# Kernel optimization log

Measured on AMD Instinct MI355X. Metric: run time of the kernel, lower is better.

The kernel has to match this reference:

```python
import jax, jax.numpy as jnp
import numpy as np

NUM_LAYER = 5
EMB_DIM = 128
N_NODES = 50000
N_EDGES = 600000
BN_EPS = 1e-5


def setup_inputs() -> dict:
    key = jax.random.key(0)
    ks = jax.random.split(key, 16)
    d, L = EMB_DIM, NUM_LAYER
    s = 0.05
    inp = {
        "x": jax.random.randint(ks[0], (N_NODES, 3), 0, 3),
        "edge_index": jax.random.randint(ks[1], (2, N_EDGES), 0, N_NODES),
        "edge_attr": jax.random.randint(ks[2], (N_EDGES, 2), 0, 4),
        # node-feature embedding tables
        "atom_emb": jax.random.normal(ks[3], (120, d)) * s,
        "chir_emb": jax.random.normal(ks[4], (3, d)) * s,
        "hyb_emb": jax.random.normal(ks[5], (7, d)) * s,
        # per-layer GIN params, stacked over layers
        "e1": jax.random.normal(ks[6], (L, 6, d)) * s,   # bond-type edge emb
        "e2": jax.random.normal(ks[7], (L, 4, d)) * s,   # bond-direction edge emb
        "W1": jax.random.normal(ks[8], (L, d, 2 * d)) * s,
        "b1": jnp.zeros((L, 2 * d)),
        "W2": jax.random.normal(ks[9], (L, 2 * d, d)) * s,
        "b2": jnp.zeros((L, d)),
        "gamma": jnp.ones((L, d)),
        "beta": jnp.zeros((L, d)),
    }
    return inp


def _gnn_forward(x, edge_index, edge_attr, atom_emb, chir_emb, hyb_emb,
                 e1, e2, W1, b1, W2, b2, gamma, beta):
    src, dst = edge_index[0], edge_index[1]
    # input node embedding: sum of three categorical embeddings -> [N, d]
    h = atom_emb[x[:, 0]] + chir_emb[x[:, 1]] + hyb_emb[x[:, 2]]
    for l in range(NUM_LAYER):
        # per-edge embedding fused from two categorical tables -> [E, d]
        ee = e1[l][edge_attr[:, 0]] + e2[l][edge_attr[:, 1]]
        # gather source features, add edge emb, scatter-add to destination
        msg = h[src] + ee                                  # [E, d]
        agg = jax.ops.segment_sum(msg, dst, num_segments=N_NODES)  # [N, d]
        # GIN MLP: Linear(d,2d) -> ReLU -> Linear(2d,d)
        h2 = jax.nn.relu(agg @ W1[l] + b1[l]) @ W2[l] + b2[l]
        # BatchNorm1d (training-mode batch statistics, biased var)
        mu = h2.mean(axis=0)
        var = h2.var(axis=0)
        h2 = gamma[l] * (h2 - mu) * jax.lax.rsqrt(var + BN_EPS) + beta[l]
        # ReLU on all but the last layer (dropout is identity in eval)
        h = h2 if l == NUM_LAYER - 1 else jax.nn.relu(h2)
    return h


def reference(x, edge_index, edge_attr, atom_emb, chir_emb, hyb_emb,
              e1, e2, W1, b1, W2, b2, gamma, beta):
    return _gnn_forward(x, edge_index, edge_attr, atom_emb, chir_emb, hyb_emb,
                        e1, e2, W1, b1, W2, b2, gamma, beta)
```

## Files before the change

kernel.cpp:

```cpp
#include <hip/hip_runtime.h>
#include <hip/hip_bf16.h>

#define NN 50000
#define NE 600000
#define D 128
#define NL 5
#define AGG_BLOCKS 2048
#define AGG_WAVES (AGG_BLOCKS * 4)

typedef __hip_bfloat16 bf16;
typedef unsigned short ushort_t;
typedef _Float16 half_t;
typedef __attribute__((ext_vector_type(8))) _Float16 half8;
typedef __attribute__((ext_vector_type(4))) _Float16 half4;
typedef __attribute__((ext_vector_type(8))) short short8;
typedef __attribute__((ext_vector_type(4))) float f32x4;
typedef __attribute__((ext_vector_type(2))) float f32x2;

__device__ __forceinline__ float b2f(bf16 v) { return __bfloat162float(v); }

__device__ __forceinline__ float loadF(const void* p, long long i, int isf32) {
    if (isf32) return ((const float*)p)[i];
    return b2f(((const bf16*)p)[i]);
}

__global__ void detect_k(const void* __restrict__ atom, int* __restrict__ flag) {
    __shared__ int vote;
    if (threadIdx.x == 0) vote = 0;
    __syncthreads();
    unsigned short u = ((const unsigned short*)atom)[threadIdx.x];
    unsigned short ex = (u >> 7) & 0xFF;
    if (ex >= 0x90) atomicOr(&vote, 1);
    __syncthreads();
    if (threadIdx.x == 0) *flag = vote;
}

__global__ void zero_f(float* __restrict__ p, int n) {
    int i = blockIdx.x * 256 + threadIdx.x;
    if (i < n) p[i] = 0.f;
}
__global__ void zero_i(int* __restrict__ p, int n) {
    int i = blockIdx.x * 256 + threadIdx.x;
    if (i < n) p[i] = 0;
}

__global__ void prepw_k(const void* __restrict__ W1, const void* __restrict__ W2,
                        const void* __restrict__ e1, const void* __restrict__ e2,
                        const int* __restrict__ fl,
                        half_t* __restrict__ w1t, half_t* __restrict__ w2t,
                        float* __restrict__ combT) {
    int isf32 = *fl;
    int idx = blockIdx.x * 256 + threadIdx.x;
    const int per = NL * 2 * D * D;
    if (idx < per) {
        int l = idx / (2 * D * D);
        int r = idx % (2 * D * D);
        int n = r >> 7, k = r & 127;
        w1t[idx] = (half_t)loadF(W1, (long long)l * 2 * D * D + (long long)k * 256 + n, isf32);
    } else if (idx < 2 * per) {
        int j = idx - per;
        int l = j / (2 * D * D);
        int r = j % (2 * D * D);
        int n = r >> 8, k = r & 255;
        w2t[j] = (half_t)loadF(W2, (long long)l * 2 * D * D + (long long)k * D + n, isf32);
    } else if (idx < 2 * per + NL * 24 * D) {
        int j = idx - 2 * per;
        int l = j / (24 * D);
        int r = j % (24 * D);
        int c = r >> 7, f = r & 127;
        combT[j] = loadF(e1, (long long)l * 6 * D + (long long)(c >> 2) * D + f, isf32) +
                   loadF(e2, (long long)l * 4 * D + (long long)(c & 3) * D + f, isf32);
    }
}

__global__ void hist_k(const int* __restrict__ ei, int* __restrict__ deg) {
    int e = blockIdx.x * 256 + threadIdx.x;
    if (e < NE) atomicAdd(&deg[ei[NE + e]], 1);
}

__global__ void scan1_k(const int* __restrict__ deg, int* __restrict__ tmp,
                        int* __restrict__ partial) {
    __shared__ int s[256];
    int t = threadIdx.x;
    int i = blockIdx.x * 256 + t;
    int v = (i < NN) ? deg[i] : 0;
    s[t] = v;
    __syncthreads();
    for (int off = 1; off < 256; off <<= 1) {
        int x = (t >= off) ? s[t - off] : 0;
        __syncthreads();
        s[t] += x;
        __syncthreads();
    }
    if (i < NN) tmp[i] = s[t];
    if (t == 255) partial[blockIdx.x] = s[255];
}

__global__ void scan2_k(int* __restrict__ partial, int nb) {
    __shared__ int s[256];
    int t = threadIdx.x;
    int v = (t < nb) ? partial[t] : 0;
    s[t] = v;
    __syncthreads();
    for (int off = 1; off < 256; off <<= 1) {
        int x = (t >= off) ? s[t - off] : 0;
        __syncthreads();
        s[t] += x;
        __syncthreads();
    }
    int excl = s[t] - v;
    __syncthreads();
    if (t < nb) partial[t] = excl;
}

__global__ void scan3_k(const int* __restrict__ tmp, const int* __restrict__ partial,
                        const int* __restrict__ deg,
                        int* __restrict__ row_start, int* __restrict__ next) {
    int i = blockIdx.x * 256 + threadIdx.x;
    if (i >= NN) return;
    int incl = tmp[i] + partial[i >> 8];
    row_start[i + 1] = incl;
    next[i] = incl - deg[i];
    if (i == 0) row_start[0] = 0;
}

__global__ void fill_k(const int* __restrict__ ei, const int* __restrict__ ea,
                       int* __restrict__ next, int* __restrict__ csr) {
    int e = blockIdx.x * 256 + threadIdx.x;
    if (e >= NE) return;
    int src = ei[e];
    int dst = ei[NE + e];
    int c = ea[2 * e] * 4 + ea[2 * e + 1];
    int pos = atomicAdd(&next[dst], 1);
    csr[pos] = src | (c << 16);
}

__global__ void embed_k(const int* __restrict__ x,
                        const void* __restrict__ atom,
                        const void* __restrict__ chir,
                        const void* __restrict__ hyb,
                        const int* __restrict__ fl,
                        half_t* __restrict__ h2) {
    int isf32 = *fl;
    int idx = blockIdx.x * 256 + threadIdx.x;
    if (idx >= NN * 64) return;
    int n = idx >> 6, fp = (idx & 63) * 2;
    long long i0 = (long long)x[n * 3 + 0] * D + fp;
    long long i1 = (long long)x[n * 3 + 1] * D + fp;
    long long i2 = (long long)x[n * 3 + 2] * D + fp;
    float v0 = loadF(atom, i0, isf32) + loadF(chir, i1, isf32) + loadF(hyb, i2, isf32);
    float v1 = loadF(atom, i0 + 1, isf32) + loadF(chir, i1 + 1, isf32) + loadF(hyb, i2 + 1, isf32);
    half_t* dst = h2 + (long long)n * D + fp;
    dst[0] = (half_t)v0;
    dst[1] = (half_t)v1;
}

__global__ void norm_k(half_t* __restrict__ h2,
                       const float* __restrict__ stats,
                       const void* __restrict__ gm, const void* __restrict__ bt,
                       const int* __restrict__ fl, int lprev) {
    __shared__ float norm_s[2 * D];
    int isf32 = *fl;
    int tid = threadIdx.x;
    if (tid < D) {
        float mu = stats[tid] * (1.f / NN);
        float var = fmaxf(stats[D + tid] * (1.f / NN) - mu * mu, 0.f);
        float rs = rsqrtf(var + 1e-5f);
        float sc = rs * loadF(gm, (long long)lprev * D + tid, isf32);
        float sh = loadF(bt, (long long)lprev * D + tid, isf32) - mu * sc;
        norm_s[tid] = sc;
        norm_s[D + tid] = sh;
    }
    __syncthreads();
    int idx = blockIdx.x * 256 + tid;
    if (idx >= NN * 16) return;
    int fp = (idx & 15) * 8;
    half_t* p = h2 + (long long)(idx >> 4) * D + fp;
    half8 v = *(half8*)p;
#pragma unroll
    for (int j = 0; j < 8; ++j) {
        float f = fmaxf(fmaf((float)v[j], norm_s[fp + j], norm_s[D + fp + j]), 0.f);
        v[j] = (half_t)f;
    }
    *(half8*)p = v;
}

__global__ __launch_bounds__(256) void aggr_k(
        const half_t* __restrict__ h,
        const int* __restrict__ row_start,
        const int* __restrict__ csr,
        const float* __restrict__ combT, int layer,
        half_t* __restrict__ agg) {
    __shared__ float comb[24 * D];
    int tid = threadIdx.x;
    const float* ct = combT + layer * 24 * D;
    for (int i = tid * 4; i < 24 * D; i += 1024)
        *(f32x4*)&comb[i] = *(const f32x4*)(ct + i);
    __syncthreads();
    int lane = tid & 63;
    int hh = lane >> 5;
    int f4 = (lane & 31) * 4;
    int wgid = blockIdx.x * 4 + (tid >> 6);
    int n0 = (int)(((long long)wgid * NN) >> 13);
    int n1 = (int)(((long long)(wgid + 1) * NN) >> 13);
    int beg = row_start[n0];
    for (int n = n0; n < n1; ++n) {
        int end = row_start[n + 1];
        f32x4 va = {0.f, 0.f, 0.f, 0.f};
        f32x4 vb = {0.f, 0.f, 0.f, 0.f};
        int i = beg;
        for (; i + 3 < end; i += 4) {
            int pkA = csr[i + hh];
            int pkB = csr[i + 2 + hh];
            half4 gA = *(const half4*)(h + (long long)(pkA & 0xFFFF) * D + f4);
            half4 gB = *(const half4*)(h + (long long)(pkB & 0xFFFF) * D + f4);
            f32x4 cA = *(const f32x4*)&comb[(pkA >> 16) * D + f4];
            f32x4 cB = *(const f32x4*)&comb[(pkB >> 16) * D + f4];
#pragma unroll
            for (int j = 0; j < 4; ++j) {
                va[j] += (float)gA[j] + cA[j];
                vb[j] += (float)gB[j] + cB[j];
            }
        }
        for (; i + 1 < end; i += 2) {
            int pk = csr[i + hh];
            half4 g = *(const half4*)(h + (long long)(pk & 0xFFFF) * D + f4);
            f32x4 c = *(const f32x4*)&comb[(pk >> 16) * D + f4];
#pragma unroll
            for (int j = 0; j < 4; ++j)
                va[j] += (float)g[j] + c[j];
        }
        if (i < end && hh == 0) {
            int pk = csr[i];
            half4 g = *(const half4*)(h + (long long)(pk & 0xFFFF) * D + f4);
            f32x4 c = *(const f32x4*)&comb[(pk >> 16) * D + f4];
#pragma unroll
            for (int j = 0; j < 4; ++j)
                va[j] += (float)g[j] + c[j];
        }
        half4 o;
#pragma unroll
        for (int j = 0; j < 4; ++j) {
            float v = va[j] + vb[j];
            v += __shfl_down(v, 32, 64);
            o[j] = (half_t)v;
        }
        if (hh == 0)
            *(half4*)(agg + (long long)n * D + f4) = o;
        beg = end;
    }
}

__global__ __launch_bounds__(512) void mlp_k(
        const half_t* __restrict__ agg,
        const half_t* __restrict__ w1t, const half_t* __restrict__ w2t,
        const void* __restrict__ b1, const void* __restrict__ b2,
        const int* __restrict__ fl, int layer,
        half_t* __restrict__ h2,
        float* __restrict__ statsAdd, float* __restrict__ statsZero) {
    __shared__ ushort_t Bs1[64 * 136];
    __shared__ ushort_t Bs2[128 * 72];
    __shared__ ushort_t Ms[128 * 72];
    __shared__ float SS[2 * D];
    int isf32 = *fl;
    int m0 = blockIdx.x * 128;
    long long b1off = (long long)layer * 2 * D;
    long long b2off = (long long)layer * D;
    int tid = threadIdx.x;
    if (blockIdx.x == 0 && tid < 2 * D) statsZero[tid] = 0.f;
    if (tid < 2 * D) SS[tid] = 0.f;
    int w = tid >> 6, lane = tid & 63;
    int quad = lane >> 4, l16 = lane & 15;

    int arow = m0 + w * 16 + l16;
    if (arow >= NN) arow = NN - 1;
    const half_t* ap = agg + (long long)arow * D + quad * 8;
    half8 afrag[4];
#pragma unroll
    for (int kk4 = 0; kk4 < 4; ++kk4)
        afrag[kk4] = *(const half8*)(ap + kk4 * 32);

    const half_t* w1p = w1t + (long long)layer * 256 * 128;
    const half_t* w2p = w2t + (long long)layer * 128 * 256;
    f32x4 acc[8];
#pragma unroll
    for (int t = 0; t < 8; ++t) acc[t] = (f32x4){0.f, 0.f, 0.f, 0.f};

    for (int nc = 0; nc < 4; ++nc) {
        __syncthreads();
        {
            int r = tid >> 3, kq = (tid & 7) * 16;
            const ushort_t* src = (const ushort_t*)(w1p + (long long)(nc * 64 + r) * 128 + kq);
            ushort_t* dst = &Bs1[r * 136 + kq];
            *(short8*)(dst) = *(const short8*)(src);
            *(short8*)(dst + 8) = *(const short8*)(src + 8);
        }
        {
            int r = tid >> 2, kq = (tid & 3) * 16;
            const ushort_t* src = (const ushort_t*)(w2p + (long long)r * 256 + nc * 64 + kq);
            ushort_t* dst = &Bs2[r * 72 + kq];
            *(short8*)(dst) = *(const short8*)(src);
            *(short8*)(dst + 8) = *(const short8*)(src + 8);
        }
        __syncthreads();
        f32x4 macc[4];
#pragma unroll
        for (int nt = 0; nt < 4; ++nt) macc[nt] = (f32x4){0.f, 0.f, 0.f, 0.f};
#pragma unroll
        for (int kk4 = 0; kk4 < 4; ++kk4) {
            half8 a = afrag[kk4];
#pragma unroll
            for (int nt = 0; nt < 4; ++nt) {
                half8 b = *(const half8*)&Bs1[(nt * 16 + l16) * 136 + kk4 * 32 + quad * 8];
                macc[nt] = __builtin_amdgcn_mfma_f32_16x16x32_f16(a, b, macc[nt], 0, 0, 0);
            }
        }
#pragma unroll
        for (int nt = 0; nt < 4; ++nt) {
            float bias = loadF(b1, b1off + nc * 64 + nt * 16 + l16, isf32);
#pragma unroll
            for (int r = 0; r < 4; ++r) {
                float v = fmaxf(macc[nt][r] + bias, 0.f);
                half_t hv = (half_t)v;
                Ms[(w * 16 + quad * 4 + r) * 72 + nt * 16 + l16] = *(ushort_t*)&hv;
            }
        }
        __syncthreads();
#pragma unroll
        for (int kk4 = 0; kk4 < 2; ++kk4) {
            half8 a = *(const half8*)&Ms[(w * 16 + l16) * 72 + kk4 * 32 + quad * 8];
#pragma unroll
            for (int t = 0; t < 8; ++t) {
                half8 b = *(const half8*)&Bs2[((t >> 2) * 64 + (t & 3) * 16 + l16) * 72 + kk4 * 32 + quad * 8];
                acc[t] = __builtin_amdgcn_mfma_f32_16x16x32_f16(a, b, acc[t], 0, 0, 0);
            }
        }
    }
#pragma unroll
    for (int t = 0; t < 8; ++t) {
        int col = (t >> 2) * 64 + (t & 3) * 16 + l16;
        float bias = loadF(b2, b2off + col, isf32);
        float s = 0.f, q = 0.f;
#pragma unroll
        for (int r = 0; r < 4; ++r) {
            int row = m0 + w * 16 + quad * 4 + r;
            if (row < NN) {
                float v = acc[t][r] + bias;
                h2[(long long)row * D + col] = (half_t)v;
                s += v; q += v * v;
            }
        }
        atomicAdd(&SS[col], s);
        atomicAdd(&SS[D + col], q);
    }
    __syncthreads();
    if (tid < 2 * D) atomicAdd(&statsAdd[tid], SS[tid]);
}

__global__ void apply_k(const half_t* __restrict__ h2,
                        const float* __restrict__ statsPrev,
                        const void* __restrict__ gm, const void* __restrict__ bt,
                        const int* __restrict__ fl,
                        float* __restrict__ out) {
    __shared__ float norm_s[2 * D];
    int isf32 = *fl;
    int tid = threadIdx.x;
    if (tid < D) {
        float mu = statsPrev[tid] * (1.f / NN);
        float var = fmaxf(statsPrev[D + tid] * (1.f / NN) - mu * mu, 0.f);
        float rs = rsqrtf(var + 1e-5f);
        float sc = rs * loadF(gm, (long long)(NL - 1) * D + tid, isf32);
        float sh = loadF(bt, (long long)(NL - 1) * D + tid, isf32) - mu * sc;
        norm_s[tid] = sc;
        norm_s[D + tid] = sh;
    }
    __syncthreads();
    int idx = blockIdx.x * 256 + tid;
    if (idx >= NN * 64) return;
    int fp = (idx & 63) * 2;
    unsigned hv = *(const unsigned*)(h2 + (long long)(idx >> 6) * D + fp);
    float v0 = fmaf((float)((const half_t*)&hv)[0], norm_s[fp], norm_s[D + fp]);
    float v1 = fmaf((float)((const half_t*)&hv)[1], norm_s[fp + 1], norm_s[D + fp + 1]);
    f32x2 o; o.x = v0; o.y = v1;
    *(f32x2*)(out + (long long)(idx >> 6) * D + fp) = o;
}

extern "C" void kernel_launch(void* const* d_in, const int* in_sizes, int n_in,
                              void* d_out, int out_size, void* d_ws, size_t ws_size,
                              hipStream_t stream) {
    const int* x     = (const int*)d_in[0];
    const int* ei    = (const int*)d_in[1];
    const int* ea    = (const int*)d_in[2];
    const void* atom = d_in[3];
    const void* chir = d_in[4];
    const void* hyb  = d_in[5];
    const void* e1   = d_in[6];
    const void* e2   = d_in[7];
    const void* W1   = d_in[8];
    const void* b1   = d_in[9];
    const void* W2   = d_in[10];
    const void* b2   = d_in[11];
    const void* gm   = d_in[12];
    const void* bt   = d_in[13];

    const size_t ND = (size_t)NN * D;

    char* base = (char*)d_ws;
    float* SP0     = (float*)base;
    float* SP1     = (float*)(base + 1024);
    int*   flag    = (int*)(base + 2048);
    char*  p       = base + 4096;
    half_t* h2     = (half_t*)p;  p += ND * 2;
    half_t* w1t    = (half_t*)p;  p += (size_t)NL * 2 * D * D * 2;
    half_t* w2t    = (half_t*)p;  p += (size_t)NL * 2 * D * D * 2;
    float* combT   = (float*)p;   p += (size_t)NL * 24 * D * 4;
    int* csr       = (int*)p;     p += (size_t)NE * 4;
    int* row_start = (int*)p;     p += (size_t)(NN + 1) * 4 + 12;
    int* deg       = (int*)p;     p += (size_t)NN * 4;
    int* tmp       = (int*)p;     p += (size_t)NN * 4;
    int* next      = (int*)p;     p += (size_t)NN * 4;
    int* partial   = (int*)p;

    half_t* aggf = (half_t*)d_out;

    const int N2_BLOCKS = (NN * 64 + 255) / 256;
    const int NRM_BLOCKS = (NN * 16 + 255) / 256;
    const int E_BLOCKS  = (NE + 255) / 256;
    const int N_BLOCKS  = (NN + 255) / 256;
    const int M_TILES   = (NN + 127) / 128;
    const int PW_BLOCKS = (2 * NL * 2 * D * D + NL * 24 * D + 255) / 256;

    detect_k<<<1, 256, 0, stream>>>(atom, flag);
    prepw_k<<<PW_BLOCKS, 256, 0, stream>>>(W1, W2, e1, e2, flag, w1t, w2t, combT);

    zero_i<<<N_BLOCKS, 256, 0, stream>>>(deg, NN);
    hist_k<<<E_BLOCKS, 256, 0, stream>>>(ei, deg);
    scan1_k<<<N_BLOCKS, 256, 0, stream>>>(deg, tmp, partial);
    scan2_k<<<1, 256, 0, stream>>>(partial, N_BLOCKS);
    scan3_k<<<N_BLOCKS, 256, 0, stream>>>(tmp, partial, deg, row_start, next);
    fill_k<<<E_BLOCKS, 256, 0, stream>>>(ei, ea, next, csr);

    embed_k<<<N2_BLOCKS, 256, 0, stream>>>(x, atom, chir, hyb, flag, h2);
    zero_f<<<2, 256, 0, stream>>>(SP0, 2 * 2 * D);

    for (int l = 0; l < NL; ++l) {
        float* sPrev = ((l - 1) & 1) ? SP1 : SP0;
        float* sAdd  = (l & 1) ? SP1 : SP0;
        float* sZero = ((l + 1) & 1) ? SP1 : SP0;
        if (l > 0)
            norm_k<<<NRM_BLOCKS, 256, 0, stream>>>(h2, sPrev, gm, bt, flag, l - 1);
        aggr_k<<<AGG_BLOCKS, 256, 0, stream>>>(h2, row_start, csr, combT, l, aggf);
        mlp_k<<<M_TILES, 512, 0, stream>>>(aggf, w1t, w2t, b1, b2, flag, l,
                                           h2, sAdd, sZero);
    }
    apply_k<<<N2_BLOCKS, 256, 0, stream>>>(h2, SP0, gm, bt, flag, (float*)d_out);
}
```

Before: 593.5 us.

## Make MLP kernel persistent with full weights resident in LDS

The MLP kernel now launches a fixed 256 blocks that loop over 128-row tiles. Each block loads the full per-layer W1 and W2 into LDS once, instead of reloading 64-column chunks every tile. Block-wide barriers between chunks become a wave-local LDS waitcnt, which is safe because each wave reads only its own rows of the intermediate buffer. BatchNorm partial sums are kept in registers across tiles and reduced with shuffles before one LDS and global atomic pass. The larger LDS footprint (about 155 KB) allows only one block per CU, and 391 tiles over 256 blocks leaves the work unevenly split.

```diff
diff --git a/kernel.cpp b/kernel.cpp
--- a/kernel.cpp
+++ b/kernel.cpp
@@ -6,7 +6,8 @@
 #define D 128
 #define NL 5
 #define AGG_BLOCKS 2048
-#define AGG_WAVES (AGG_BLOCKS * 4)
+#define M_TILES 391
+#define MLP_BLOCKS 256
 
 typedef __hip_bfloat16 bf16;
 typedef unsigned short ushort_t;
@@ -258,103 +259,126 @@
         const int* __restrict__ fl, int layer,
         half_t* __restrict__ h2,
         float* __restrict__ statsAdd, float* __restrict__ statsZero) {
-    __shared__ ushort_t Bs1[64 * 136];
-    __shared__ ushort_t Bs2[128 * 72];
+    __shared__ ushort_t Bs1[256 * 136];
+    __shared__ ushort_t Bs2[128 * 264];
     __shared__ ushort_t Ms[128 * 72];
-    __shared__ float SS[2 * D];
     int isf32 = *fl;
-    int m0 = blockIdx.x * 128;
+    int tid = threadIdx.x;
+    if (blockIdx.x == 0 && tid < 2 * D) statsZero[tid] = 0.f;
+
+    const half_t* w1p = w1t + (long long)layer * 256 * 128;
+    const half_t* w2p = w2t + (long long)layer * 128 * 256;
+    for (int i = tid; i < 256 * 8; i += 512) {
+        int r = i >> 3, kq = (i & 7) * 16;
+        const ushort_t* src = (const ushort_t*)w1p + r * 128 + kq;
+        ushort_t* dst = &Bs1[r * 136 + kq];
+        *(short8*)dst = *(const short8*)src;
+        *(short8*)(dst + 8) = *(const short8*)(src + 8);
+    }
+    for (int i = tid; i < 128 * 16; i += 512) {
+        int r = i >> 4, kq = (i & 15) * 16;
+        const ushort_t* src = (const ushort_t*)w2p + r * 256 + kq;
+        ushort_t* dst = &Bs2[r * 264 + kq];
+        *(short8*)dst = *(const short8*)src;
+        *(short8*)(dst + 8) = *(const short8*)(src + 8);
+    }
+    __syncthreads();
+
+    int w = tid >> 6, lane = tid & 63;
+    int quad = lane >> 4, l16 = lane & 15;
     long long b1off = (long long)layer * 2 * D;
     long long b2off = (long long)layer * D;
-    int tid = threadIdx.x;
-    if (blockIdx.x == 0 && tid < 2 * D) statsZero[tid] = 0.f;
-    if (tid < 2 * D) SS[tid] = 0.f;
-    int w = tid >> 6, lane = tid & 63;
-    int quad = lane >> 4, l16 = lane & 15;
-
-    int arow = m0 + w * 16 + l16;
-    if (arow >= NN) arow = NN - 1;
-    const half_t* ap = agg + (long long)arow * D + quad * 8;
-    half8 afrag[4];
-#pragma unroll
-    for (int kk4 = 0; kk4 < 4; ++kk4)
-        afrag[kk4] = *(const half8*)(ap + kk4 * 32);
-
-    const half_t* w1p = w1t + (long long)layer * 256 * 128;
-    const half_t* w2p = w2t + (long long)layer * 128 * 256;
-    f32x4 acc[8];
-#pragma unroll
-    for (int t = 0; t < 8; ++t) acc[t] = (f32x4){0.f, 0.f, 0.f, 0.f};
-
-    for (int nc = 0; nc < 4; ++nc) {
-        __syncthreads();
-        {
-            int r = tid >> 3, kq = (tid & 7) * 16;
-            const ushort_t* src = (const ushort_t*)(w1p + (long long)(nc * 64 + r) * 128 + kq);
-            ushort_t* dst = &Bs1[r * 136 + kq];
-            *(short8*)(dst) = *(const short8*)(src);
-            *(short8*)(dst + 8) = *(const short8*)(src + 8);
-        }
-        {
-            int r = tid >> 2, kq = (tid & 3) * 16;
-            const ushort_t* src = (const ushort_t*)(w2p + (long long)r * 256 + nc * 64 + kq);
-            ushort_t* dst = &Bs2[r * 72 + kq];
-            *(short8*)(dst) = *(const short8*)(src);
-            *(short8*)(dst + 8) = *(const short8*)(src + 8);
-        }
-        __syncthreads();
-        f32x4 macc[4];
-#pragma unroll
-        for (int nt = 0; nt < 4; ++nt) macc[nt] = (f32x4){0.f, 0.f, 0.f, 0.f};
-#pragma unroll
-        for (int kk4 = 0; kk4 < 4; ++kk4) {
-            half8 a = afrag[kk4];
+
+    float ssum[8], sq[8];
+#pragma unroll
+    for (int t = 0; t < 8; ++t) { ssum[t] = 0.f; sq[t] = 0.f; }
+
+    for (int tile = blockIdx.x; tile < M_TILES; tile += MLP_BLOCKS) {
+        int m0 = tile * 128;
+        int arow = m0 + w * 16 + l16;
+        if (arow >= NN) arow = NN - 1;
+        const half_t* ap = agg + (long long)arow * D + quad * 8;
+        half8 afrag[4];
+#pragma unroll
+        for (int kk4 = 0; kk4 < 4; ++kk4)
+            afrag[kk4] = *(const half8*)(ap + kk4 * 32);
+
+        f32x4 acc[8];
+#pragma unroll
+        for (int t = 0; t < 8; ++t) acc[t] = (f32x4){0.f, 0.f, 0.f, 0.f};
+
+#pragma unroll
+        for (int nc = 0; nc < 4; ++nc) {
+            f32x4 macc[4];
+#pragma unroll
+            for (int nt = 0; nt < 4; ++nt) macc[nt] = (f32x4){0.f, 0.f, 0.f, 0.f};
+#pragma unroll
+            for (int kk4 = 0; kk4 < 4; ++kk4) {
+                half8 a = afrag[kk4];
+#pragma unroll
+                for (int nt = 0; nt < 4; ++nt) {
+                    half8 b = *(const half8*)&Bs1[(nc * 64 + nt * 16 + l16) * 136 + kk4 * 32 + quad * 8];
+                    macc[nt] = __builtin_amdgcn_mfma_f32_16x16x32_f16(a, b, macc[nt], 0, 0, 0);
+                }
+            }
 #pragma unroll
             for (int nt = 0; nt < 4; ++nt) {
-                half8 b = *(const half8*)&Bs1[(nt * 16 + l16) * 136 + kk4 * 32 + quad * 8];
-                macc[nt] = __builtin_amdgcn_mfma_f32_16x16x32_f16(a, b, macc[nt], 0, 0, 0);
+                float bias = loadF(b1, b1off + nc * 64 + nt * 16 + l16, isf32);
+#pragma unroll
+                for (int r = 0; r < 4; ++r) {
+                    float v = fmaxf(macc[nt][r] + bias, 0.f);
+                    half_t hv = (half_t)v;
+                    Ms[(w * 16 + quad * 4 + r) * 72 + nt * 16 + l16] = *(ushort_t*)&hv;
+                }
             }
-        }
-#pragma unroll
-        for (int nt = 0; nt < 4; ++nt) {
-            float bias = loadF(b1, b1off + nc * 64 + nt * 16 + l16, isf32);
+            asm volatile("s_waitcnt lgkmcnt(0)" ::: "memory");
+#pragma unroll
+            for (int kk4 = 0; kk4 < 2; ++kk4) {
+                half8 a = *(const half8*)&Ms[(w * 16 + l16) * 72 + kk4 * 32 + quad * 8];
+#pragma unroll
+                for (int t = 0; t < 8; ++t) {
+                    half8 b = *(const half8*)&Bs2[((t >> 2) * 64 + (t & 3) * 16 + l16) * 264 + nc * 64 + kk4 * 32 + quad * 8];
+                    acc[t] = __builtin_amdgcn_mfma_f32_16x16x32_f16(a, b, acc[t], 0, 0, 0);
+                }
+            }
+        }
+#pragma unroll
+        for (int t = 0; t < 8; ++t) {
+            int col = (t >> 2) * 64 + (t & 3) * 16 + l16;
+            float bias = loadF(b2, b2off + col, isf32);
 #pragma unroll
             for (int r = 0; r < 4; ++r) {
-                float v = fmaxf(macc[nt][r] + bias, 0.f);
-                half_t hv = (half_t)v;
-                Ms[(w * 16 + quad * 4 + r) * 72 + nt * 16 + l16] = *(ushort_t*)&hv;
+                int row = m0 + w * 16 + quad * 4 + r;
+                if (row < NN) {
+                    float v = acc[t][r] + bias;
+                    h2[(long long)row * D + col] = (half_t)v;
+                    ssum[t] += v; sq[t] += v * v;
+                }
             }
         }
-        __syncthreads();
-#pragma unroll
-        for (int kk4 = 0; kk4 < 2; ++kk4) {
-            half8 a = *(const half8*)&Ms[(w * 16 + l16) * 72 + kk4 * 32 + quad * 8];
-#pragma unroll
-            for (int t = 0; t < 8; ++t) {
-                half8 b = *(const half8*)&Bs2[((t >> 2) * 64 + (t & 3) * 16 + l16) * 72 + kk4 * 32 + quad * 8];
-                acc[t] = __builtin_amdgcn_mfma_f32_16x16x32_f16(a, b, acc[t], 0, 0, 0);
-            }
-        }
-    }
+    }
+
 #pragma unroll
     for (int t = 0; t < 8; ++t) {
-        int col = (t >> 2) * 64 + (t & 3) * 16 + l16;
-        float bias = loadF(b2, b2off + col, isf32);
-        float s = 0.f, q = 0.f;
-#pragma unroll
-        for (int r = 0; r < 4; ++r) {
-            int row = m0 + w * 16 + quad * 4 + r;
-            if (row < NN) {
-                float v = acc[t][r] + bias;
-                h2[(long long)row * D + col] = (half_t)v;
-                s += v; q += v * v;
-            }
-        }
-        atomicAdd(&SS[col], s);
-        atomicAdd(&SS[D + col], q);
-    }
-    __syncthreads();
-    if (tid < 2 * D) atomicAdd(&statsAdd[tid], SS[tid]);
+        ssum[t] += __shfl_xor(ssum[t], 16, 64);
+        ssum[t] += __shfl_xor(ssum[t], 32, 64);
+        sq[t]   += __shfl_xor(sq[t], 16, 64);
+        sq[t]   += __shfl_xor(sq[t], 32, 64);
+    }
+    __syncthreads();
+    float* SSf = (float*)Ms;
+    if (tid < 2 * D) SSf[tid] = 0.f;
+    __syncthreads();
+    if (quad == 0) {
+#pragma unroll
+        for (int t = 0; t < 8; ++t) {
+            int col = (t >> 2) * 64 + (t & 3) * 16 + l16;
+            atomicAdd(&SSf[col], ssum[t]);
+            atomicAdd(&SSf[D + col], sq[t]);
+        }
+    }
+    __syncthreads();
+    if (tid < 2 * D) atomicAdd(&statsAdd[tid], SSf[tid]);
 }
 
 __global__ void apply_k(const half_t* __restrict__ h2,
@@ -427,7 +451,6 @@
     const int NRM_BLOCKS = (NN * 16 + 255) / 256;
     const int E_BLOCKS  = (NE + 255) / 256;
     const int N_BLOCKS  = (NN + 255) / 256;
-    const int M_TILES   = (NN + 127) / 128;
     const int PW_BLOCKS = (2 * NL * 2 * D * D + NL * 24 * D + 255) / 256;
 
     detect_k<<<1, 256, 0, stream>>>(atom, flag);
@@ -450,8 +473,8 @@
         if (l > 0)
             norm_k<<<NRM_BLOCKS, 256, 0, stream>>>(h2, sPrev, gm, bt, flag, l - 1);
         aggr_k<<<AGG_BLOCKS, 256, 0, stream>>>(h2, row_start, csr, combT, l, aggf);
-        mlp_k<<<M_TILES, 512, 0, stream>>>(aggf, w1t, w2t, b1, b2, flag, l,
-                                           h2, sAdd, sZero);
+        mlp_k<<<MLP_BLOCKS, 512, 0, stream>>>(aggf, w1t, w2t, b1, b2, flag, l,
+                                              h2, sAdd, sZero);
     }
     apply_k<<<N2_BLOCKS, 256, 0, stream>>>(h2, SP0, gm, bt, flag, (float*)d_out);
 }
```

New measurement: 540.3 us. 1.1x faster.
